# Kernel tuning notes

Hardware: AMD Instinct MI355X
Metric: run time of the kernel (lower is better)

The kernel has to match this reference:

```python
import jax, jax.numpy as jnp
import numpy as np

B, N, C = 4, 2048, 1024
HEADS, DHEAD = 16, 64
EPS = 1e-7
SCALE = DHEAD ** (-0.5)


def setup_inputs() -> dict:
    key = jax.random.key(0)
    k1, k2, k3, k4 = jax.random.split(key, 4)
    inner = HEADS * DHEAD
    return {
        "x": jax.random.normal(k1, (B, N, C), dtype=jnp.float32),
        "gamma": jnp.ones((1, 1, C), dtype=jnp.float32),
        "Wq": jax.random.normal(k2, (inner, C), dtype=jnp.float32) * np.sqrt(1.0 / C),
        "Wkv": jax.random.normal(k3, (2 * DHEAD, C), dtype=jnp.float32) * np.sqrt(1.0 / C),
        "Wo": jax.random.normal(k4, (C, inner), dtype=jnp.float32) * np.sqrt(1.0 / inner) * 1e-5,
        "ls_scale": jnp.full((C,), 1e-4, dtype=jnp.float32),
    }


def reference(x, gamma, Wq, Wkv, Wo, ls_scale):
    # BiasFreeLayerNorm: divide by unbiased std (no mean subtraction), scale by gamma
    std = jnp.std(x, axis=-1, ddof=1, keepdims=True)
    xn = (x / (std + EPS)) * gamma
    # q from normalized x, k/v from the ORIGINAL x (kv_input = x before norm)
    q = xn @ Wq.T                       # [B, N, H*D]
    kv = x @ Wkv.T                      # [B, N, 2*D]
    k, v = kv[..., :DHEAD], kv[..., DHEAD:]  # shared single kv head (MQA)
    q = q.reshape(B, N, HEADS, DHEAD).transpose(0, 2, 1, 3) * SCALE  # [B, H, N, D]
    sim = jnp.einsum('bhid,bjd->bhij', q, k)
    attn = jax.nn.softmax(sim, axis=-1)
    out = jnp.einsum('bhij,bjd->bhid', attn, v)       # [B, H, N, D]
    out = out.transpose(0, 2, 1, 3).reshape(B, N, HEADS * DHEAD)
    out = out @ Wo.T
    return ls_scale * out
```

## Files before the change

### kernel.cpp

```cpp
#include <hip/hip_runtime.h>
#include <hip/hip_bf16.h>
#include <stdint.h>

typedef __attribute__((ext_vector_type(8))) short short8;
typedef __attribute__((ext_vector_type(4))) short short4v;
typedef __attribute__((ext_vector_type(4))) float f32x4;
typedef __attribute__((ext_vector_type(4))) unsigned short us4;

#define B_ 4
#define N_ 2048
#define C_ 1024
#define H_ 16
#define D_ 64

__device__ __forceinline__ unsigned short f2bf(float f) {
  union { float f; unsigned u; } v; v.f = f;
  unsigned u = v.u;
  u += 0x7fffu + ((u >> 16) & 1u);
  return (unsigned short)(u >> 16);
}

__device__ __forceinline__ unsigned short bfc(float f) {
  union { __hip_bfloat16 h; unsigned short u; } v;
  v.h = __float2bfloat16(f);
  return v.u;
}

__device__ __forceinline__ void glds16(const unsigned short* g, const unsigned short* l) {
  __builtin_amdgcn_global_load_lds(
      (const __attribute__((address_space(1))) void*)(uintptr_t)g,
      (__attribute__((address_space(3))) void*)(uintptr_t)l, 16, 0, 0);
}

__device__ __forceinline__ f32x4 mfma16(short8 a, short8 b, f32x4 c) {
  return __builtin_amdgcn_mfma_f32_16x16x32_bf16(a, b, c, 0, 0, 0);
}

#if __has_builtin(__builtin_amdgcn_mfma_f32_16x16x16bf16_1k)
__device__ __forceinline__ f32x4 mfma16b(short4v a, short4v b, f32x4 c) {
  return __builtin_amdgcn_mfma_f32_16x16x16bf16_1k(a, b, c, 0, 0, 0);
}
#else
__device__ __forceinline__ f32x4 mfma16b(short4v a, short4v b, f32x4 c) {
  asm volatile("v_mfma_f32_16x16x16_bf16 %0, %1, %2, %0\n\ts_nop 7\n\ts_nop 7"
               : "+v"(c) : "v"(a), "v"(b));
  return c;
}
#endif

__global__ __launch_bounds__(256) void prep_cast_k(const float* __restrict__ x,
                                                   const float* __restrict__ gamma,
                                                   unsigned short* __restrict__ xb,
                                                   float* __restrict__ rstd_v,
                                                   const float* __restrict__ wq,
                                                   const float* __restrict__ wkv,
                                                   const float* __restrict__ wo,
                                                   unsigned short* __restrict__ dq,
                                                   unsigned short* __restrict__ dkv,
                                                   unsigned short* __restrict__ dwo) {
  const int t = threadIdx.x;
  if (blockIdx.x >= 8192) {
    const int i = (blockIdx.x - 8192) * 256 + t;
    if (i < 262144) {
      const float4 v = ((const float4*)wq)[i];
      const float4 gv = ((const float4*)gamma)[i & 255];
      us4 o;
      o.x = f2bf(v.x * gv.x); o.y = f2bf(v.y * gv.y);
      o.z = f2bf(v.z * gv.z); o.w = f2bf(v.w * gv.w);
      ((us4*)dq)[i] = o;
    } else {
      const float* s;
      unsigned short* d;
      int j;
      if (i < 294912) { s = wkv; d = dkv; j = i - 262144; }
      else { s = wo; d = dwo; j = i - 294912; }
      const float4 v = ((const float4*)s)[j];
      us4 o; o.x = f2bf(v.x); o.y = f2bf(v.y); o.z = f2bf(v.z); o.w = f2bf(v.w);
      ((us4*)d)[j] = o;
    }
    return;
  }
  const int row = blockIdx.x;
  const float4 v = ((const float4*)(x + (size_t)row * C_))[t];
  float s1 = v.x + v.y + v.z + v.w;
  float s2 = v.x * v.x + v.y * v.y + v.z * v.z + v.w * v.w;
#pragma unroll
  for (int off = 32; off > 0; off >>= 1) {
    s1 += __shfl_down(s1, off);
    s2 += __shfl_down(s2, off);
  }
  __shared__ float r1[4], r2[4];
  if ((t & 63) == 0) { r1[t >> 6] = s1; r2[t >> 6] = s2; }
  __syncthreads();
  s1 = r1[0] + r1[1] + r1[2] + r1[3];
  s2 = r2[0] + r2[1] + r2[2] + r2[3];
  const float var = (s2 - s1 * s1 * (1.0f / C_)) * (1.0f / (C_ - 1));
  const float rstd = 1.0f / (sqrtf(var) + 1e-7f);
  if (t == 0) rstd_v[row] = rstd;
  us4 a;
  a.x = f2bf(v.x); a.y = f2bf(v.y); a.z = f2bf(v.z); a.w = f2bf(v.w);
  ((us4*)(xb + (size_t)row * C_))[t] = a;
}

__global__ __launch_bounds__(256, 2) void qkv_gemm(const unsigned short* __restrict__ xb,
                                                   const unsigned short* __restrict__ wq,
                                                   const unsigned short* __restrict__ wkv,
                                                   const float* __restrict__ rstd_v,
                                                   unsigned short* __restrict__ qo,
                                                   unsigned short* __restrict__ kvo,
                                                   unsigned short* __restrict__ vtb) {
  const bool iskv = (blockIdx.x == 8);
  const unsigned short* Bw = iskv ? wkv : wq;
  const int n0 = iskv ? 0 : blockIdx.x * 128;
  const int K = 1024, m0 = blockIdx.y * 128;

  __shared__ unsigned short At[128 * 32];
  __shared__ unsigned short Bt[128 * 32];
  const int t = threadIdx.x;
  const int w = t >> 6, l = t & 63;
  const int ql = l & 15, g = l >> 4;
  const int wr = (w >> 1) * 64, wc = (w & 1) * 64;

  const int pr0 = t >> 2, pb0 = t & 3;
  const int lb0 = pb0 ^ ((pr0 >> 1) & 3);
  const int pr1 = 64 + (t >> 2);
  const int lb1 = pb0 ^ ((pr1 >> 1) & 3);
  const unsigned short* Ab = xb + (size_t)m0 * K;
  const unsigned short* Bb = Bw + (size_t)n0 * K;

  f32x4 acc[4][4];
#pragma unroll
  for (int i = 0; i < 4; ++i)
#pragma unroll
    for (int j = 0; j < 4; ++j) acc[i][j] = f32x4{0.f, 0.f, 0.f, 0.f};

  for (int k0 = 0; k0 < K; k0 += 32) {
    glds16(Ab + (size_t)pr0 * K + k0 + lb0 * 8, &At[w * 512]);
    glds16(Ab + (size_t)pr1 * K + k0 + lb1 * 8, &At[2048 + w * 512]);
    glds16(Bb + (size_t)pr0 * K + k0 + lb0 * 8, &Bt[w * 512]);
    glds16(Bb + (size_t)pr1 * K + k0 + lb1 * 8, &Bt[2048 + w * 512]);
    __syncthreads();
    short8 af[4], bfr[4];
#pragma unroll
    for (int i = 0; i < 4; ++i) {
      const int row = wr + i * 16 + ql;
      af[i] = *(const short8*)&At[row * 32 + ((g ^ ((row >> 1) & 3)) * 8)];
    }
#pragma unroll
    for (int i = 0; i < 4; ++i) {
      const int row = wc + i * 16 + ql;
      bfr[i] = *(const short8*)&Bt[row * 32 + ((g ^ ((row >> 1) & 3)) * 8)];
    }
#pragma unroll
    for (int mi = 0; mi < 4; ++mi)
#pragma unroll
      for (int ni = 0; ni < 4; ++ni)
        acc[mi][ni] = mfma16(af[mi], bfr[ni], acc[mi][ni]);
    __syncthreads();
  }

  if (!iskv) {
    float rs[4][4];
#pragma unroll
    for (int mi = 0; mi < 4; ++mi)
#pragma unroll
      for (int r = 0; r < 4; ++r)
        rs[mi][r] = 0.18033688011112042f * rstd_v[m0 + wr + mi * 16 + g * 4 + r];
#pragma unroll
    for (int mi = 0; mi < 4; ++mi)
#pragma unroll
      for (int ni = 0; ni < 4; ++ni) {
        const int col = n0 + wc + ni * 16 + ql;
#pragma unroll
        for (int r = 0; r < 4; ++r) {
          const int row = m0 + wr + mi * 16 + g * 4 + r;
          qo[(size_t)row * 1024 + col] = f2bf(acc[mi][ni][r] * rs[mi][r]);
        }
      }
  } else if (wc == 0) {
#pragma unroll
    for (int mi = 0; mi < 4; ++mi)
#pragma unroll
      for (int ni = 0; ni < 4; ++ni) {
        const int col = ni * 16 + ql;
#pragma unroll
        for (int r = 0; r < 4; ++r) {
          const int row = m0 + wr + mi * 16 + g * 4 + r;
          kvo[(size_t)row * 128 + col] = f2bf(acc[mi][ni][r]);
        }
      }
  } else {
    const int brow = m0 >> 11;
    unsigned short* vb = vtb + (size_t)brow * 64 * 2048;
#pragma unroll
    for (int mi = 0; mi < 4; ++mi) {
      const int nbase = (m0 & 2047) + wr + mi * 16 + g * 4;
#pragma unroll
      for (int ni = 0; ni < 4; ++ni) {
        const int d = ni * 16 + ql;
        const int nadj = nbase ^ (((d >> 3) & 1) ? 4 : 0);
        us4 st;
        st.x = f2bf(acc[mi][ni][0]);
        st.y = f2bf(acc[mi][ni][1]);
        st.z = f2bf(acc[mi][ni][2]);
        st.w = f2bf(acc[mi][ni][3]);
        *(us4*)&vb[(size_t)d * 2048 + nadj] = st;
      }
    }
  }
}

__global__ __launch_bounds__(256, 2) void gemm_o(const unsigned short* __restrict__ A,
                                                 const unsigned short* __restrict__ Bw,
                                                 float* __restrict__ Cout,
                                                 const float* __restrict__ colscale,
                                                 int M, int N, int K) {
  __shared__ unsigned short At[128 * 32];
  __shared__ unsigned short Bt[128 * 32];
  const int t = threadIdx.x;
  const int w = t >> 6, l = t & 63;
  const int ql = l & 15, g = l >> 4;
  const int wr = (w >> 1) * 64, wc = (w & 1) * 64;
  const int m0 = blockIdx.y * 128, n0 = blockIdx.x * 128;

  const int pr0 = t >> 2, pb0 = t & 3;
  const int lb0 = pb0 ^ ((pr0 >> 1) & 3);
  const int pr1 = 64 + (t >> 2);
  const int lb1 = pb0 ^ ((pr1 >> 1) & 3);
  const unsigned short* Ab = A + (size_t)m0 * K;
  const unsigned short* Bb = Bw + (size_t)n0 * K;

  f32x4 acc[4][4];
#pragma unroll
  for (int i = 0; i < 4; ++i)
#pragma unroll
    for (int j = 0; j < 4; ++j) acc[i][j] = f32x4{0.f, 0.f, 0.f, 0.f};

  for (int k0 = 0; k0 < K; k0 += 32) {
    glds16(Ab + (size_t)pr0 * K + k0 + lb0 * 8, &At[w * 512]);
    glds16(Ab + (size_t)pr1 * K + k0 + lb1 * 8, &At[2048 + w * 512]);
    glds16(Bb + (size_t)pr0 * K + k0 + lb0 * 8, &Bt[w * 512]);
    glds16(Bb + (size_t)pr1 * K + k0 + lb1 * 8, &Bt[2048 + w * 512]);
    __syncthreads();
    short8 af[4], bfr[4];
#pragma unroll
    for (int i = 0; i < 4; ++i) {
      const int row = wr + i * 16 + ql;
      af[i] = *(const short8*)&At[row * 32 + ((g ^ ((row >> 1) & 3)) * 8)];
    }
#pragma unroll
    for (int i = 0; i < 4; ++i) {
      const int row = wc + i * 16 + ql;
      bfr[i] = *(const short8*)&Bt[row * 32 + ((g ^ ((row >> 1) & 3)) * 8)];
    }
#pragma unroll
    for (int mi = 0; mi < 4; ++mi)
#pragma unroll
      for (int ni = 0; ni < 4; ++ni)
        acc[mi][ni] = mfma16(af[mi], bfr[ni], acc[mi][ni]);
    __syncthreads();
  }

#pragma unroll
  for (int mi = 0; mi < 4; ++mi)
#pragma unroll
    for (int ni = 0; ni < 4; ++ni) {
      const int col = n0 + wc + ni * 16 + ql;
      const float cs = colscale[col];
#pragma unroll
      for (int r = 0; r < 4; ++r) {
        const int row = m0 + wr + mi * 16 + g * 4 + r;
        Cout[(size_t)row * N + col] = acc[mi][ni][r] * cs;
      }
    }
}

__global__ __launch_bounds__(512, 4) void attn_k(const unsigned short* __restrict__ qb,
                                                 const unsigned short* __restrict__ kvb,
                                                 const unsigned short* __restrict__ vtb,
                                                 unsigned short* __restrict__ ao) {
  __shared__ unsigned short Kt[2][64 * 64];
  __shared__ unsigned short Vt[2][64 * 64];

  const int idx = blockIdx.x;
  const int qc = idx & 15, hd = (idx >> 4) & 15, b = idx >> 8;
  const int t = threadIdx.x, w = t >> 6, l = t & 63;
  const int ql = l & 15, g = l >> 4;
  const int q0 = qc * 128 + w * 16;

  const unsigned short* qbase = qb + (size_t)(b * N_ + q0) * C_ + hd * D_;
  short8 Qf[2];
#pragma unroll
  for (int h = 0; h < 2; ++h)
    Qf[h] = *(const short8*)(qbase + (size_t)ql * C_ + 32 * h + 8 * g);

  const unsigned short* kvrow = kvb + (size_t)(b * N_) * 128;
  const unsigned short* vtrow = vtb + (size_t)b * 64 * 2048;
  const int sr = l >> 3;
  const int blk = ((l & 7) ^ sr) << 3;
  const int row0 = 8 * w + sr;
  const int sw = ql & 7;
  const int hb = (ql >> 3) & 1;

  auto stage = [&](int bi, int kt) {
    glds16(kvrow + (size_t)(kt * 64 + row0) * 128 + blk, &Kt[bi][w * 512]);
    glds16(vtrow + (size_t)row0 * 2048 + kt * 64 + blk, &Vt[bi][w * 512]);
  };

  f32x4 o[4];
#pragma unroll
  for (int dt = 0; dt < 4; ++dt) o[dt] = f32x4{0.f, 0.f, 0.f, 0.f};
  float lsum = 0.f;

  auto tilec = [&](int bi) {
    short8 Kf[4][2];
#pragma unroll
    for (int c = 0; c < 4; ++c) {
      const int roff = (16 * c + ql) * 64;
      Kf[c][0] = *(const short8*)&Kt[bi][roff + ((g ^ sw) << 3)];
      Kf[c][1] = *(const short8*)&Kt[bi][roff + (((g + 4) ^ sw) << 3)];
    }
    f32x4 s[4];
#pragma unroll
    for (int c = 0; c < 4; ++c) {
      f32x4 acc = {0.f, 0.f, 0.f, 0.f};
      acc = mfma16(Kf[c][0], Qf[0], acc);
      acc = mfma16(Kf[c][1], Qf[1], acc);
      s[c] = acc;
    }
    short4v pa[4];
    float ps = 0.f;
#pragma unroll
    for (int c = 0; c < 4; ++c) {
      const float p0 = __builtin_amdgcn_exp2f(s[c][0]);
      const float p1 = __builtin_amdgcn_exp2f(s[c][1]);
      const float p2 = __builtin_amdgcn_exp2f(s[c][2]);
      const float p3 = __builtin_amdgcn_exp2f(s[c][3]);
      ps += (p0 + p1) + (p2 + p3);
      short4v pv;
      pv[0] = (short)bfc(p0); pv[1] = (short)bfc(p1);
      pv[2] = (short)bfc(p2); pv[3] = (short)bfc(p3);
      pa[c] = pv;
    }
    lsum += ps;

    __builtin_amdgcn_s_setprio(1);
#pragma unroll
    for (int dt = 0; dt < 4; ++dt) {
      const int vro = (16 * dt + ql) * 64 + 4 * ((g & 1) ^ hb);
      short4v Vf[4];
#pragma unroll
      for (int c = 0; c < 4; ++c)
        Vf[c] = *(const short4v*)&Vt[bi][vro + (((2 * c + (g >> 1)) ^ sw) << 3)];
#pragma unroll
      for (int c = 0; c < 4; ++c)
        o[dt] = mfma16b(Vf[c], pa[c], o[dt]);
    }
    __builtin_amdgcn_s_setprio(0);
  };

  stage(0, 0);
  for (int kt = 0; kt < 32; kt += 2) {
    __syncthreads();
    stage(1, kt + 1);
    tilec(0);
    __syncthreads();
    if (kt + 2 < 32) stage(0, kt + 2);
    tilec(1);
  }

  lsum += __shfl_xor(lsum, 16);
  lsum += __shfl_xor(lsum, 32);

  const float inv = 1.0f / lsum;
  unsigned short* orow = ao + (size_t)(b * N_ + q0 + ql) * C_ + hd * D_;
#pragma unroll
  for (int dt = 0; dt < 4; ++dt) {
    us4 st;
    st.x = bfc(o[dt][0] * inv);
    st.y = bfc(o[dt][1] * inv);
    st.z = bfc(o[dt][2] * inv);
    st.w = bfc(o[dt][3] * inv);
    *(us4*)(orow + dt * 16 + 4 * g) = st;
  }
}

extern "C" void kernel_launch(void* const* d_in, const int* in_sizes, int n_in,
                              void* d_out, int out_size, void* d_ws, size_t ws_size,
                              hipStream_t stream) {
  const float* x = (const float*)d_in[0];
  const float* gamma = (const float*)d_in[1];
  const float* Wq = (const float*)d_in[2];
  const float* Wkv = (const float*)d_in[3];
  const float* Wo = (const float*)d_in[4];
  const float* ls = (const float*)d_in[5];
  float* out = (float*)d_out;

  unsigned short* ws = (unsigned short*)d_ws;
  const size_t R = (size_t)B_ * N_;
  unsigned short* xb = ws;
  unsigned short* qbuf = xb + R * C_;
  unsigned short* kvb = qbuf + R * C_;
  unsigned short* aob = kvb + R * 128;
  unsigned short* wqb = aob + R * C_;
  unsigned short* wkvb = wqb + (size_t)C_ * C_;
  unsigned short* wob = wkvb + (size_t)128 * C_;
  unsigned short* vtb = wob + (size_t)C_ * C_;
  float* rstd = (float*)(vtb + (size_t)4 * 64 * 2048);

  prep_cast_k<<<(int)R + 2176, 256, 0, stream>>>(x, gamma, xb, rstd,
                                                 Wq, Wkv, Wo, wqb, wkvb, wob);
  qkv_gemm<<<dim3(9, R / 128), 256, 0, stream>>>(xb, wqb, wkvb, rstd,
                                                 qbuf, kvb, vtb);
  attn_k<<<B_ * H_ * (N_ / 128), 512, 0, stream>>>(qbuf, kvb, vtb, aob);
  gemm_o<<<dim3(C_ / 128, R / 128), 256, 0, stream>>>(aob, wob, out, ls,
                                                      (int)R, C_, C_);
}
```

Baseline: 164.4 us.

## Switch attention to 32x32x16 MFMA with permlane swap for P operand

Rewrites the attention kernel to use 32x32x16 bf16 MFMA for both QK^T and PV, with each wave handling 32 query rows and 4 waves per block instead of 8 waves of 16 rows. The P matrix is packed to bf16 and redistributed across lane halves with v_permlane32_swap, so it can feed the PV MFMA directly without going through LDS. The V-transpose store drops its XOR swizzle to match the new LDS read pattern. Larger MFMA tiles should cut LDS fragment reads and instruction count per FLOP, at the cost of more accumulator registers and fewer waves per block.

```diff
diff --git a/kernel.cpp b/kernel.cpp
--- a/kernel.cpp
+++ b/kernel.cpp
@@ -3,8 +3,8 @@
 #include <stdint.h>
 
 typedef __attribute__((ext_vector_type(8))) short short8;
-typedef __attribute__((ext_vector_type(4))) short short4v;
 typedef __attribute__((ext_vector_type(4))) float f32x4;
+typedef __attribute__((ext_vector_type(16))) float f32x16;
 typedef __attribute__((ext_vector_type(4))) unsigned short us4;
 
 #define B_ 4
@@ -26,6 +26,14 @@
   return v.u;
 }
 
+__device__ __forceinline__ unsigned pk2(float lo, float hi) {
+  return ((unsigned)bfc(hi) << 16) | (unsigned)bfc(lo);
+}
+
+__device__ __forceinline__ void pswap(unsigned& a, unsigned& b) {
+  asm("v_permlane32_swap_b32 %0, %1" : "+v"(a), "+v"(b));
+}
+
 __device__ __forceinline__ void glds16(const unsigned short* g, const unsigned short* l) {
   __builtin_amdgcn_global_load_lds(
       (const __attribute__((address_space(1))) void*)(uintptr_t)g,
@@ -36,17 +44,9 @@
   return __builtin_amdgcn_mfma_f32_16x16x32_bf16(a, b, c, 0, 0, 0);
 }
 
-#if __has_builtin(__builtin_amdgcn_mfma_f32_16x16x16bf16_1k)
-__device__ __forceinline__ f32x4 mfma16b(short4v a, short4v b, f32x4 c) {
-  return __builtin_amdgcn_mfma_f32_16x16x16bf16_1k(a, b, c, 0, 0, 0);
-}
-#else
-__device__ __forceinline__ f32x4 mfma16b(short4v a, short4v b, f32x4 c) {
-  asm volatile("v_mfma_f32_16x16x16_bf16 %0, %1, %2, %0\n\ts_nop 7\n\ts_nop 7"
-               : "+v"(c) : "v"(a), "v"(b));
-  return c;
-}
-#endif
+__device__ __forceinline__ f32x16 mfma32(short8 a, short8 b, f32x16 c) {
+  return __builtin_amdgcn_mfma_f32_32x32x16_bf16(a, b, c, 0, 0, 0);
+}
 
 __global__ __launch_bounds__(256) void prep_cast_k(const float* __restrict__ x,
                                                    const float* __restrict__ gamma,
@@ -198,13 +198,12 @@
 #pragma unroll
       for (int ni = 0; ni < 4; ++ni) {
         const int d = ni * 16 + ql;
-        const int nadj = nbase ^ (((d >> 3) & 1) ? 4 : 0);
         us4 st;
         st.x = f2bf(acc[mi][ni][0]);
         st.y = f2bf(acc[mi][ni][1]);
         st.z = f2bf(acc[mi][ni][2]);
         st.w = f2bf(acc[mi][ni][3]);
-        *(us4*)&vb[(size_t)d * 2048 + nadj] = st;
+        *(us4*)&vb[(size_t)d * 2048 + nbase] = st;
       }
     }
   }
@@ -275,7 +274,7 @@
     }
 }
 
-__global__ __launch_bounds__(512, 4) void attn_k(const unsigned short* __restrict__ qb,
+__global__ __launch_bounds__(256, 3) void attn_k(const unsigned short* __restrict__ qb,
                                                  const unsigned short* __restrict__ kvb,
                                                  const unsigned short* __restrict__ vtb,
                                                  unsigned short* __restrict__ ao) {
@@ -285,76 +284,82 @@
   const int idx = blockIdx.x;
   const int qc = idx & 15, hd = (idx >> 4) & 15, b = idx >> 8;
   const int t = threadIdx.x, w = t >> 6, l = t & 63;
-  const int ql = l & 15, g = l >> 4;
-  const int q0 = qc * 128 + w * 16;
-
-  const unsigned short* qbase = qb + (size_t)(b * N_ + q0) * C_ + hd * D_;
-  short8 Qf[2];
-#pragma unroll
-  for (int h = 0; h < 2; ++h)
-    Qf[h] = *(const short8*)(qbase + (size_t)ql * C_ + 32 * h + 8 * g);
+  const int l31 = l & 31, hi = l >> 5, sw = l & 7;
+  const int q0 = qc * 128 + w * 32;
+
+  const unsigned short* qrow = qb + (size_t)(b * N_ + q0 + l31) * C_ + hd * D_;
+  short8 Qf[4];
+#pragma unroll
+  for (int ks = 0; ks < 4; ++ks)
+    Qf[ks] = *(const short8*)(qrow + 16 * ks + 8 * hi);
 
   const unsigned short* kvrow = kvb + (size_t)(b * N_) * 128;
   const unsigned short* vtrow = vtb + (size_t)b * 64 * 2048;
   const int sr = l >> 3;
   const int blk = ((l & 7) ^ sr) << 3;
-  const int row0 = 8 * w + sr;
-  const int sw = ql & 7;
-  const int hb = (ql >> 3) & 1;
+  const int row0 = 16 * w + sr;
+  const int row1 = row0 + 8;
 
   auto stage = [&](int bi, int kt) {
-    glds16(kvrow + (size_t)(kt * 64 + row0) * 128 + blk, &Kt[bi][w * 512]);
-    glds16(vtrow + (size_t)row0 * 2048 + kt * 64 + blk, &Vt[bi][w * 512]);
+    glds16(kvrow + (size_t)(kt * 64 + row0) * 128 + blk, &Kt[bi][(2 * w) * 512]);
+    glds16(kvrow + (size_t)(kt * 64 + row1) * 128 + blk, &Kt[bi][(2 * w + 1) * 512]);
+    glds16(vtrow + (size_t)row0 * 2048 + kt * 64 + blk, &Vt[bi][(2 * w) * 512]);
+    glds16(vtrow + (size_t)row1 * 2048 + kt * 64 + blk, &Vt[bi][(2 * w + 1) * 512]);
   };
 
-  f32x4 o[4];
-#pragma unroll
-  for (int dt = 0; dt < 4; ++dt) o[dt] = f32x4{0.f, 0.f, 0.f, 0.f};
+  f32x16 o[2];
+#pragma unroll
+  for (int dh = 0; dh < 2; ++dh)
+#pragma unroll
+    for (int r = 0; r < 16; ++r) o[dh][r] = 0.f;
   float lsum = 0.f;
 
   auto tilec = [&](int bi) {
-    short8 Kf[4][2];
-#pragma unroll
-    for (int c = 0; c < 4; ++c) {
-      const int roff = (16 * c + ql) * 64;
-      Kf[c][0] = *(const short8*)&Kt[bi][roff + ((g ^ sw) << 3)];
-      Kf[c][1] = *(const short8*)&Kt[bi][roff + (((g + 4) ^ sw) << 3)];
-    }
-    f32x4 s[4];
-#pragma unroll
-    for (int c = 0; c < 4; ++c) {
-      f32x4 acc = {0.f, 0.f, 0.f, 0.f};
-      acc = mfma16(Kf[c][0], Qf[0], acc);
-      acc = mfma16(Kf[c][1], Qf[1], acc);
-      s[c] = acc;
-    }
-    short4v pa[4];
-    float ps = 0.f;
-#pragma unroll
-    for (int c = 0; c < 4; ++c) {
-      const float p0 = __builtin_amdgcn_exp2f(s[c][0]);
-      const float p1 = __builtin_amdgcn_exp2f(s[c][1]);
-      const float p2 = __builtin_amdgcn_exp2f(s[c][2]);
-      const float p3 = __builtin_amdgcn_exp2f(s[c][3]);
-      ps += (p0 + p1) + (p2 + p3);
-      short4v pv;
-      pv[0] = (short)bfc(p0); pv[1] = (short)bfc(p1);
-      pv[2] = (short)bfc(p2); pv[3] = (short)bfc(p3);
-      pa[c] = pv;
-    }
-    lsum += ps;
+    short8 Pf[4];
+#pragma unroll
+    for (int half = 0; half < 2; ++half) {
+      const int kro = (32 * half + l31) * 64;
+      short8 Kf[4];
+#pragma unroll
+      for (int ks = 0; ks < 4; ++ks)
+        Kf[ks] = *(const short8*)&Kt[bi][kro + (((2 * ks + hi) ^ sw) << 3)];
+      f32x16 s;
+#pragma unroll
+      for (int r = 0; r < 16; ++r) s[r] = 0.f;
+#pragma unroll
+      for (int ks = 0; ks < 4; ++ks) s = mfma32(Kf[ks], Qf[ks], s);
+#pragma unroll
+      for (int w2 = 0; w2 < 2; ++w2) {
+        const float p0 = __builtin_amdgcn_exp2f(s[8 * w2 + 0]);
+        const float p1 = __builtin_amdgcn_exp2f(s[8 * w2 + 1]);
+        const float p2 = __builtin_amdgcn_exp2f(s[8 * w2 + 2]);
+        const float p3 = __builtin_amdgcn_exp2f(s[8 * w2 + 3]);
+        const float p4 = __builtin_amdgcn_exp2f(s[8 * w2 + 4]);
+        const float p5 = __builtin_amdgcn_exp2f(s[8 * w2 + 5]);
+        const float p6 = __builtin_amdgcn_exp2f(s[8 * w2 + 6]);
+        const float p7 = __builtin_amdgcn_exp2f(s[8 * w2 + 7]);
+        lsum += ((p0 + p1) + (p2 + p3)) + ((p4 + p5) + (p6 + p7));
+        unsigned a0 = pk2(p0, p1), a1 = pk2(p2, p3);
+        unsigned b0 = pk2(p4, p5), b1 = pk2(p6, p7);
+        pswap(a0, b0);
+        pswap(a1, b1);
+        union { unsigned u[4]; short8 v; } cv;
+        cv.u[0] = a0; cv.u[1] = a1; cv.u[2] = b0; cv.u[3] = b1;
+        Pf[2 * half + w2] = cv.v;
+      }
+    }
 
     __builtin_amdgcn_s_setprio(1);
 #pragma unroll
-    for (int dt = 0; dt < 4; ++dt) {
-      const int vro = (16 * dt + ql) * 64 + 4 * ((g & 1) ^ hb);
-      short4v Vf[4];
-#pragma unroll
-      for (int c = 0; c < 4; ++c)
-        Vf[c] = *(const short4v*)&Vt[bi][vro + (((2 * c + (g >> 1)) ^ sw) << 3)];
-#pragma unroll
-      for (int c = 0; c < 4; ++c)
-        o[dt] = mfma16b(Vf[c], pa[c], o[dt]);
+    for (int dh = 0; dh < 2; ++dh) {
+      const int vro = (32 * dh + l31) * 64;
+      short8 Vf[4];
+#pragma unroll
+      for (int win = 0; win < 4; ++win)
+        Vf[win] = *(const short8*)&Vt[bi][vro + (((2 * win + hi) ^ sw) << 3)];
+#pragma unroll
+      for (int win = 0; win < 4; ++win)
+        o[dh] = mfma32(Vf[win], Pf[win], o[dh]);
     }
     __builtin_amdgcn_s_setprio(0);
   };
@@ -369,20 +374,21 @@
     tilec(1);
   }
 
-  lsum += __shfl_xor(lsum, 16);
   lsum += __shfl_xor(lsum, 32);
-
   const float inv = 1.0f / lsum;
-  unsigned short* orow = ao + (size_t)(b * N_ + q0 + ql) * C_ + hd * D_;
-#pragma unroll
-  for (int dt = 0; dt < 4; ++dt) {
-    us4 st;
-    st.x = bfc(o[dt][0] * inv);
-    st.y = bfc(o[dt][1] * inv);
-    st.z = bfc(o[dt][2] * inv);
-    st.w = bfc(o[dt][3] * inv);
-    *(us4*)(orow + dt * 16 + 4 * g) = st;
-  }
+
+  unsigned short* orow = ao + (size_t)(b * N_ + q0 + l31) * C_ + hd * D_;
+#pragma unroll
+  for (int dh = 0; dh < 2; ++dh)
+#pragma unroll
+    for (int r2 = 0; r2 < 4; ++r2) {
+      us4 st;
+      st.x = bfc(o[dh][4 * r2 + 0] * inv);
+      st.y = bfc(o[dh][4 * r2 + 1] * inv);
+      st.z = bfc(o[dh][4 * r2 + 2] * inv);
+      st.w = bfc(o[dh][4 * r2 + 3] * inv);
+      *(us4*)(orow + 32 * dh + 8 * r2 + 4 * hi) = st;
+    }
 }
 
 extern "C" void kernel_launch(void* const* d_in, const int* in_sizes, int n_in,
@@ -412,7 +418,7 @@
                                                  Wq, Wkv, Wo, wqb, wkvb, wob);
   qkv_gemm<<<dim3(9, R / 128), 256, 0, stream>>>(xb, wqb, wkvb, rstd,
                                                  qbuf, kvb, vtb);
-  attn_k<<<B_ * H_ * (N_ / 128), 512, 0, stream>>>(qbuf, kvb, vtb, aob);
+  attn_k<<<B_ * H_ * (N_ / 128), 256, 0, stream>>>(qbuf, kvb, vtb, aob);
   gemm_o<<<dim3(C_ / 128, R / 128), 256, 0, stream>>>(aob, wob, out, ls,
                                                       (int)R, C_, C_);
 }
```

Result: faster. 161.0 us (-2.1%).
